# Performance work log

Measured on AMD Instinct MI355X. Metric: run time of the kernel, lower is better.

## Reference

```python
import jax, jax.numpy as jnp
import numpy as np

ALPHA = 0.2          # LeakyReLU negative slope
NEG_FILL = -9e15     # mask value used by the original module


def setup_inputs() -> dict:
    key = jax.random.key(0)
    k1, k2, k3, k4 = jax.random.split(key, 4)
    N, D, H, F = 4096, 512, 8, 64  # nhid*nheads == embedding_dim
    h = jax.random.normal(k1, (N, D), dtype=jnp.float32)
    adj = jax.random.randint(k2, (N, N), 0, 2, dtype=jnp.int32)
    # per-head linear projection weights (no bias) and attention vectors
    W = jax.random.normal(k3, (H, D, F), dtype=jnp.float32) * (1.0 / np.sqrt(D))
    a = jax.random.normal(k4, (H, 2 * F), dtype=jnp.float32) * 0.1
    return {"h": h, "adj": adj, "W": W, "a": a}


def reference(h, adj, W, a):
    H, D, F = W.shape
    N = h.shape[0]
    # per-head projection: [H, N, F]
    hp = jnp.einsum('nd,hdf->hnf', h, W)
    # score(i,j) = leakyrelu(a[:F].h_i + a[F:].h_j)  (decomposed broadcast-add,
    # same math as the original N*N concat construction)
    a_src, a_dst = a[:, :F], a[:, F:]
    f_src = jnp.einsum('hnf,hf->hn', hp, a_src)  # [H, N]
    f_dst = jnp.einsum('hnf,hf->hn', hp, a_dst)  # [H, N]
    e = jax.nn.leaky_relu(f_src[:, :, None] + f_dst[:, None, :], ALPHA)  # [H,N,N]
    e = jnp.where(adj[None] > 0, e, NEG_FILL)
    att = jax.nn.softmax(e, axis=-1)  # softmax over neighbors j (dim=1 in torch)
    out = jnp.einsum('hij,hjf->hif', att, hp)  # [H, N, F]
    # concat heads -> [N, H*F], then ELU
    out = jnp.transpose(out, (1, 0, 2)).reshape(N, H * F)
    return jax.nn.elu(out)
```

## Files before the change

### kernel.cpp

```cpp
#include <hip/hip_runtime.h>

#define NN 4096
#define DD 512
#define HH 8
#define FF 64
#define LRELU_ALPHA 0.2f
#define SP 72

typedef __attribute__((ext_vector_type(8))) short bf16x8;
typedef __attribute__((ext_vector_type(4))) float f32x4;

__device__ __forceinline__ float f4c(const float4& v, int k) {
    return k == 0 ? v.x : (k == 1 ? v.y : (k == 2 ? v.z : v.w));
}
__device__ __forceinline__ void f4s(float4& v, int k, float x) {
    if (k == 0) v.x = x; else if (k == 1) v.y = x; else if (k == 2) v.z = x; else v.w = x;
}
__device__ __forceinline__ unsigned short f2bf(float x) {
    unsigned u = __float_as_uint(x);
    return (unsigned short)((u + 0x7fffu + ((u >> 16) & 1u)) >> 16);
}
__device__ __forceinline__ float bf2f(unsigned short h) {
    return __uint_as_float(((unsigned)h) << 16);
}
__device__ __forceinline__ unsigned fkey(float x) {
    unsigned u = __float_as_uint(x);
    return (u & 0x80000000u) ? ~u : (u | 0x80000000u);
}
__device__ __forceinline__ float funkey(unsigned k) {
    unsigned u = (k & 0x80000000u) ? (k ^ 0x80000000u) : ~k;
    return __uint_as_float(u);
}

__global__ __launch_bounds__(256) void k_prep(const int* __restrict__ adj,
                                              const float* __restrict__ W,
                                              unsigned* __restrict__ adjw,
                                              unsigned short* __restrict__ wt_hi,
                                              unsigned short* __restrict__ wt_lo,
                                              unsigned* __restrict__ mxkey,
                                              float* __restrict__ hpsum) {
    __shared__ float tile[64][65];
    int b = blockIdx.x, t = threadIdx.x;
    if (b < 4096) {
        int lane = t & 63;
        #pragma unroll
        for (int i = 0; i < 16; i++) {
            int tid = ((b * 16 + i) << 8) + t;
            unsigned long long mask = __ballot(adj[tid] > 0);
            if (lane == 0) {
                int base = tid >> 5;
                adjw[base] = (unsigned)mask;
                adjw[base + 1] = (unsigned)(mask >> 32);
            }
        }
    } else if (b < 4160) {
        int idx = b - 4096;
        int h = idx >> 3;
        int d0 = (idx & 7) * 64;
        #pragma unroll
        for (int kidx = 0; kidx < 4; kidx++) {
            int id = t + 256 * kidx;
            int dd = id >> 4, f4i = (id & 15) * 4;
            float4 v = *(const float4*)(W + ((size_t)(h * DD + d0 + dd)) * FF + f4i);
            tile[dd][f4i] = v.x; tile[dd][f4i + 1] = v.y;
            tile[dd][f4i + 2] = v.z; tile[dd][f4i + 3] = v.w;
        }
        __syncthreads();
        int f = t >> 2, c = (t & 3) * 16;
        union { unsigned short s[16]; uint4 v[2]; } hb, lb;
        #pragma unroll
        for (int q = 0; q < 16; q++) {
            float v = tile[c + q][f];
            unsigned short hi = f2bf(v);
            hb.s[q] = hi;
            lb.s[q] = f2bf(v - bf2f(hi));
        }
        uint4* dh = (uint4*)(wt_hi + ((size_t)h * FF + f) * DD + d0 + c);
        uint4* dl = (uint4*)(wt_lo + ((size_t)h * FF + f) * DD + d0 + c);
        dh[0] = hb.v[0]; dh[1] = hb.v[1];
        dl[0] = lb.v[0]; dl[1] = lb.v[1];
    } else {
        if (t < 16) mxkey[t] = 0u;
        hpsum[t] = 0.f;
        hpsum[t + 256] = 0.f;
    }
}

__global__ __launch_bounds__(256) void k_hp_mfma(const float* __restrict__ hmat,
                                                 const unsigned short* __restrict__ whi,
                                                 const unsigned short* __restrict__ wlo,
                                                 const float* __restrict__ a,
                                                 unsigned short* __restrict__ hpT_hi,
                                                 float* __restrict__ fs,
                                                 float* __restrict__ fd,
                                                 float* __restrict__ hpsum,
                                                 unsigned* __restrict__ mxkey) {
    __shared__ char smem[4 * 64 * SP * 2];
    unsigned short* ah = (unsigned short*)smem;
    unsigned short* al = ah + 64 * SP;
    unsigned short* bh = al + 64 * SP;
    unsigned short* bl = bh + 64 * SP;

    int t = threadIdx.x;
    int h = blockIdx.y;
    int n0 = blockIdx.x * 64;
    int lane = t & 63;
    int w = t >> 6;
    int R0 = (w >> 1) * 32, F0 = (w & 1) * 32;
    int am = lane & 15, aq = lane >> 4;
    int sr = t >> 2, sc = (t & 3) * 16;

    const float* gha = hmat + (size_t)(n0 + sr) * DD;
    const unsigned short* gbh = whi + ((size_t)h * FF + sr) * DD;
    const unsigned short* gbl = wlo + ((size_t)h * FF + sr) * DD;

    f32x4 acc[2][2] = {};
    for (int kk = 0; kk < DD; kk += 64) {
        {
            float4 p0 = *(const float4*)(gha + kk + sc);
            float4 p1 = *(const float4*)(gha + kk + sc + 4);
            float4 p2 = *(const float4*)(gha + kk + sc + 8);
            float4 p3 = *(const float4*)(gha + kk + sc + 12);
            union { unsigned short s[16]; uint4 v[2]; } hb, lb;
            #pragma unroll
            for (int q = 0; q < 16; q++) {
                float v = q < 4 ? f4c(p0, q) : q < 8 ? f4c(p1, q - 4)
                          : q < 12 ? f4c(p2, q - 8) : f4c(p3, q - 12);
                unsigned short hi = f2bf(v);
                hb.s[q] = hi;
                lb.s[q] = f2bf(v - bf2f(hi));
            }
            *(uint4*)(ah + sr * SP + sc) = hb.v[0]; *(uint4*)(ah + sr * SP + sc + 8) = hb.v[1];
            *(uint4*)(al + sr * SP + sc) = lb.v[0]; *(uint4*)(al + sr * SP + sc + 8) = lb.v[1];
        }
        {
            const uint4* s2 = (const uint4*)(gbh + kk + sc);
            const uint4* s3 = (const uint4*)(gbl + kk + sc);
            uint4 w0 = s2[0], w1 = s2[1], x0 = s3[0], x1 = s3[1];
            *(uint4*)(bh + sr * SP + sc) = w0; *(uint4*)(bh + sr * SP + sc + 8) = w1;
            *(uint4*)(bl + sr * SP + sc) = x0; *(uint4*)(bl + sr * SP + sc + 8) = x1;
        }
        __syncthreads();
        #pragma unroll
        for (int k2 = 0; k2 < 2; k2++) {
            int ko = k2 * 32 + aq * 8;
            bf16x8 a0h = *(const bf16x8*)(ah + (R0 + am) * SP + ko);
            bf16x8 a1h = *(const bf16x8*)(ah + (R0 + 16 + am) * SP + ko);
            bf16x8 a0l = *(const bf16x8*)(al + (R0 + am) * SP + ko);
            bf16x8 a1l = *(const bf16x8*)(al + (R0 + 16 + am) * SP + ko);
            bf16x8 b0h = *(const bf16x8*)(bh + (F0 + am) * SP + ko);
            bf16x8 b1h = *(const bf16x8*)(bh + (F0 + 16 + am) * SP + ko);
            bf16x8 b0l = *(const bf16x8*)(bl + (F0 + am) * SP + ko);
            bf16x8 b1l = *(const bf16x8*)(bl + (F0 + 16 + am) * SP + ko);
            acc[0][0] = __builtin_amdgcn_mfma_f32_16x16x32_bf16(a0h, b0h, acc[0][0], 0, 0, 0);
            acc[0][1] = __builtin_amdgcn_mfma_f32_16x16x32_bf16(a0h, b1h, acc[0][1], 0, 0, 0);
            acc[1][0] = __builtin_amdgcn_mfma_f32_16x16x32_bf16(a1h, b0h, acc[1][0], 0, 0, 0);
            acc[1][1] = __builtin_amdgcn_mfma_f32_16x16x32_bf16(a1h, b1h, acc[1][1], 0, 0, 0);
            acc[0][0] = __builtin_amdgcn_mfma_f32_16x16x32_bf16(a0h, b0l, acc[0][0], 0, 0, 0);
            acc[0][1] = __builtin_amdgcn_mfma_f32_16x16x32_bf16(a0h, b1l, acc[0][1], 0, 0, 0);
            acc[1][0] = __builtin_amdgcn_mfma_f32_16x16x32_bf16(a1h, b0l, acc[1][0], 0, 0, 0);
            acc[1][1] = __builtin_amdgcn_mfma_f32_16x16x32_bf16(a1h, b1l, acc[1][1], 0, 0, 0);
            acc[0][0] = __builtin_amdgcn_mfma_f32_16x16x32_bf16(a0l, b0h, acc[0][0], 0, 0, 0);
            acc[0][1] = __builtin_amdgcn_mfma_f32_16x16x32_bf16(a0l, b1h, acc[0][1], 0, 0, 0);
            acc[1][0] = __builtin_amdgcn_mfma_f32_16x16x32_bf16(a1l, b0h, acc[1][0], 0, 0, 0);
            acc[1][1] = __builtin_amdgcn_mfma_f32_16x16x32_bf16(a1l, b1h, acc[1][1], 0, 0, 0);
        }
        __syncthreads();
    }

    unsigned* tt = (unsigned*)smem;
    float* rs = (float*)(smem + 17408);
    float* rd = rs + 256;
    float* ash = rd + 256;
    if (t < 128) ash[t] = a[h * 2 * FF + t];
    int col = lane & 15, rbase = (lane >> 4) * 4;
    #pragma unroll
    for (int m16 = 0; m16 < 2; m16++) {
        #pragma unroll
        for (int n16 = 0; n16 < 2; n16++) {
            #pragma unroll
            for (int r = 0; r < 4; r++) {
                int nl = R0 + m16 * 16 + rbase + r;
                int f = F0 + n16 * 16 + col;
                float v = acc[m16][n16][r];
                unsigned short hi = f2bf(v);
                unsigned short lo = f2bf(v - bf2f(hi));
                tt[f * 68 + nl] = (unsigned)hi | ((unsigned)lo << 16);
            }
        }
    }
    __syncthreads();
    {
        int f = t >> 2, c = (t & 3) * 16;
        union { unsigned short s[16]; uint4 v[2]; } hb;
        float csum = 0.f;
        #pragma unroll
        for (int q = 0; q < 16; q++) {
            unsigned u = tt[f * 68 + c + q];
            hb.s[q] = (unsigned short)(u & 0xffffu);
            csum += bf2f((unsigned short)(u & 0xffffu)) + bf2f((unsigned short)(u >> 16));
        }
        uint4* dh = (uint4*)(hpT_hi + ((size_t)h * FF + f) * NN + n0 + c);
        dh[0] = hb.v[0]; dh[1] = hb.v[1];
        csum += __shfl_xor(csum, 1);
        csum += __shfl_xor(csum, 2);
        if ((t & 3) == 0) unsafeAtomicAdd(hpsum + h * FF + f, csum);
    }
    {
        int n = t & 63, g = t >> 6;
        float fsp = 0.f, fdp = 0.f;
        #pragma unroll
        for (int q = 0; q < 16; q++) {
            int f = g * 16 + q;
            unsigned u = tt[f * 68 + n];
            float v = bf2f((unsigned short)(u & 0xffffu)) + bf2f((unsigned short)(u >> 16));
            fsp += v * ash[f];
            fdp += v * ash[64 + f];
        }
        rs[g * 64 + n] = fsp;
        rd[g * 64 + n] = fdp;
    }
    __syncthreads();
    if (t < 64) {
        float fdv = rd[t] + rd[64 + t] + rd[128 + t] + rd[192 + t];
        fs[(size_t)h * NN + n0 + t] = rs[t] + rs[64 + t] + rs[128 + t] + rs[192 + t];
        fd[(size_t)h * NN + n0 + t] = fdv;
        unsigned key = fkey(fdv);
        #pragma unroll
        for (int off = 32; off; off >>= 1) key = max(key, (unsigned)__shfl_xor((int)key, off));
        if (t == 0) atomicMax(mxkey + h, key);
    }
}

__global__ __launch_bounds__(256) void k_attn(const float* __restrict__ fs,
                                              const float* __restrict__ fd,
                                              const unsigned* __restrict__ mxkey,
                                              const unsigned* __restrict__ adjw,
                                              const unsigned short* __restrict__ hpT_hi,
                                              const float* __restrict__ hpsum,
                                              float* __restrict__ outp) {
    __shared__ unsigned short pa[2][32 * SP];
    __shared__ unsigned short hbh[2][64 * SP];
    __shared__ float fss[32], ms[32];

    int t = threadIdx.x;
    int h = blockIdx.y;
    int i0 = blockIdx.x * 32;
    int lane = t & 63;
    int w = t >> 6;

    const float LOG2E = 1.44269504f;
    float mfd = funkey(mxkey[h]);
    if (t < 32) {
        float fsv = fs[(size_t)h * NN + i0 + t];
        fss[t] = fsv;
        float s = fsv + mfd;
        float m = fmaxf(s, LRELU_ALPHA * s);
        ms[t] = m * LOG2E;
    }
    __syncthreads();

    int wr = t >> 3;
    int wc = (t & 7) * 8;
    int sr = t >> 2, sc = (t & 3) * 16;
    int R0 = (w >> 1) * 16, F0 = (w & 1) * 32;
    int am = lane & 15, aq = lane >> 4;
    f32x4 acc[2] = {};
    f32x4 accl = {};
    bf16x8 bones;
    #pragma unroll
    for (int i = 0; i < 8; i++) bones[i] = (short)0x3f80;

    const unsigned short* gH = hpT_hi + (size_t)h * FF * NN;
    const float* fdh = fd + (size_t)h * NN;
    float fsr = fss[wr], mr = ms[wr];

    auto produce = [&](int j0, int buf) {
        {
            const uint4* sh = (const uint4*)(gH + (size_t)sr * NN + j0 + sc);
            uint4 v0 = sh[0], v1 = sh[1];
            *(uint4*)(&hbh[buf][sr * SP + sc]) = v0;
            *(uint4*)(&hbh[buf][sr * SP + sc + 8]) = v1;
        }
        {
            unsigned word = adjw[(size_t)(i0 + wr) * (NN / 32) + ((j0 + wc) >> 5)];
            unsigned bits = word >> (wc & 31);
            union { unsigned u[4]; uint4 v; } wb;
            #pragma unroll
            for (int q = 0; q < 2; q++) {
                float4 fdv = *(const float4*)(fdh + j0 + wc + q * 4);
                unsigned eu[4];
                #pragma unroll
                for (int b = 0; b < 4; b++) {
                    float s = fsr + f4c(fdv, b);
                    float l = fmaxf(s, LRELU_ALPHA * s);
                    float e = __builtin_amdgcn_exp2f(__builtin_fmaf(l, LOG2E, -mr));
                    e = ((bits >> (q * 4 + b)) & 1u) ? e : 0.f;
                    eu[b] = __float_as_uint(e);
                }
                wb.u[q * 2]     = __builtin_amdgcn_perm(eu[1], eu[0], 0x07060302);
                wb.u[q * 2 + 1] = __builtin_amdgcn_perm(eu[3], eu[2], 0x07060302);
            }
            *(uint4*)(&pa[buf][wr * SP + wc]) = wb.v;
        }
    };

    produce(0, 0);
    __syncthreads();
    for (int j0 = 0; j0 < NN; j0 += 64) {
        int cur = (j0 >> 6) & 1;
        if (j0 + 64 < NN) produce(j0 + 64, cur ^ 1);
        #pragma unroll
        for (int k2 = 0; k2 < 2; k2++) {
            int ko = k2 * 32 + aq * 8;
            bf16x8 a0 = *(const bf16x8*)(&pa[cur][(R0 + am) * SP + ko]);
            bf16x8 b0 = *(const bf16x8*)(&hbh[cur][(F0 + am) * SP + ko]);
            bf16x8 b1 = *(const bf16x8*)(&hbh[cur][(F0 + 16 + am) * SP + ko]);
            acc[0] = __builtin_amdgcn_mfma_f32_16x16x32_bf16(a0, b0, acc[0], 0, 0, 0);
            acc[1] = __builtin_amdgcn_mfma_f32_16x16x32_bf16(a0, b1, acc[1], 0, 0, 0);
            accl   = __builtin_amdgcn_mfma_f32_16x16x32_bf16(a0, bones, accl, 0, 0, 0);
        }
        __syncthreads();
    }

    const float invN = 1.0f / NN;
    int col = lane & 15, rbase = (lane >> 4) * 4;
    #pragma unroll
    for (int r = 0; r < 4; r++) {
        int row = i0 + R0 + rbase + r;
        float l = accl[r];
        float rl = 1.f / l;
        #pragma unroll
        for (int n16 = 0; n16 < 2; n16++) {
            int f = F0 + n16 * 16 + col;
            float v;
            if (l > 0.f) v = acc[n16][r] * rl;
            else         v = hpsum[h * FF + f] * invN;
            v = v > 0.f ? v : __expf(v) - 1.f;
            outp[(size_t)row * (HH * FF) + h * FF + f] = v;
        }
    }
}

extern "C" void kernel_launch(void* const* d_in, const int* in_sizes, int n_in,
                              void* d_out, int out_size, void* d_ws, size_t ws_size,
                              hipStream_t stream) {
    const float* hmat = (const float*)d_in[0];
    const int*   adj  = (const int*)d_in[1];
    const float* W    = (const float*)d_in[2];
    const float* a    = (const float*)d_in[3];
    float* out = (float*)d_out;

    char* ws = (char*)d_ws;
    unsigned short* hpT_hi = (unsigned short*)(ws);
    unsigned*       adjw   = (unsigned*)(ws + (4u << 20));
    unsigned short* wt_hi  = (unsigned short*)(ws + (6u << 20));
    unsigned short* wt_lo  = (unsigned short*)(ws + (6u << 20) + (512u << 10));
    float* fs    = (float*)(ws + (7u << 20));
    float* fd    = (float*)(ws + (7u << 20) + (128u << 10));
    unsigned* mxkey = (unsigned*)(ws + (7u << 20) + (256u << 10));
    float* hpsum = (float*)(mxkey + 16);

    k_prep   <<<dim3(4161),          256, 0, stream>>>(adj, W, adjw, wt_hi, wt_lo,
                                                       mxkey, hpsum);
    k_hp_mfma<<<dim3(64, 8),         256, 0, stream>>>(hmat, wt_hi, wt_lo, a,
                                                       hpT_hi, fs, fd, hpsum, mxkey);
    k_attn   <<<dim3(NN / 32, HH),   256, 0, stream>>>(fs, fd, mxkey, adjw,
                                                       hpT_hi, hpsum, out);
}
```

Baseline: 192.0 us.

## Build P fragments in registers with scalar wave-wide adjacency masks

The adjacency bitmask is repacked in the prep kernel into per-wave 64-bit lane masks matching the MFMA fragment layout. The attention kernel then computes the exp-weight fragment directly in registers, with the mask applied as an SGPR operand to v_cndmask. This removes the shared-memory P buffer. LOG2E is folded into fs/fd upstream, and the LeakyReLU/max subtraction is rewritten as precomputed per-row constants. Each block now covers 64 rows, with every wave computing all 64 features, and output is written as float4. The cost is a more complex mask transpose in prep and higher register pressure from holding 16 mask words per iteration.

Result: slower. 219.5 us (+14.3%).

```diff
diff --git a/kernel.cpp b/kernel.cpp
--- a/kernel.cpp
+++ b/kernel.cpp
@@ -34,27 +34,42 @@
 
 __global__ __launch_bounds__(256) void k_prep(const int* __restrict__ adj,
                                               const float* __restrict__ W,
-                                              unsigned* __restrict__ adjw,
+                                              unsigned long long* __restrict__ adjm,
                                               unsigned short* __restrict__ wt_hi,
                                               unsigned short* __restrict__ wt_lo,
                                               unsigned* __restrict__ mxkey,
                                               float* __restrict__ hpsum) {
-    __shared__ float tile[64][65];
+    __shared__ unsigned long long shbuf[2080];
     int b = blockIdx.x, t = threadIdx.x;
-    if (b < 4096) {
-        int lane = t & 63;
-        #pragma unroll
-        for (int i = 0; i < 16; i++) {
-            int tid = ((b * 16 + i) << 8) + t;
-            unsigned long long mask = __ballot(adj[tid] > 0);
-            if (lane == 0) {
-                int base = tid >> 5;
-                adjw[base] = (unsigned)mask;
-                adjw[base + 1] = (unsigned)(mask >> 32);
+    if (b < 1024) {
+        int g = b >> 2, cq = b & 3;
+        int r0 = g * 16;
+        int lane = t & 63, wv = t >> 6;
+        unsigned long long (*w64)[17] = (unsigned long long(*)[17])shbuf;
+        for (int r = 0; r < 16; r++) {
+            #pragma unroll
+            for (int q = 0; q < 4; q++) {
+                int col = cq * 1024 + q * 256 + t;
+                unsigned long long m = __ballot(adj[(size_t)(r0 + r) * NN + col] > 0);
+                if (lane == 0) w64[r][q * 4 + wv] = m;
             }
         }
-    } else if (b < 4160) {
-        int idx = b - 4096;
+        __syncthreads();
+        for (int tt = wv; tt < 16; tt += 4) {
+            unsigned long long wbits = w64[lane & 15][tt];
+            unsigned long long my = 0;
+            #pragma unroll
+            for (int k = 0; k < 16; k++) {
+                int shv = 32 * (k >> 3) + 8 * (lane >> 4) + (k & 7);
+                unsigned long long bal = __ballot((unsigned)((wbits >> shv) & 1ULL));
+                if (lane == k) my = bal;
+            }
+            if (lane < 16)
+                adjm[((size_t)g * 64 + cq * 16 + tt) * 16 + lane] = my;
+        }
+    } else if (b < 1088) {
+        float (*tile)[65] = (float(*)[65])shbuf;
+        int idx = b - 1024;
         int h = idx >> 3;
         int d0 = (idx & 7) * 64;
         #pragma unroll
@@ -222,8 +237,9 @@
     }
     __syncthreads();
     if (t < 64) {
-        float fdv = rd[t] + rd[64 + t] + rd[128 + t] + rd[192 + t];
-        fs[(size_t)h * NN + n0 + t] = rs[t] + rs[64 + t] + rs[128 + t] + rs[192 + t];
+        const float LOG2E = 1.44269504f;
+        float fdv = (rd[t] + rd[64 + t] + rd[128 + t] + rd[192 + t]) * LOG2E;
+        fs[(size_t)h * NN + n0 + t] = (rs[t] + rs[64 + t] + rs[128 + t] + rs[192 + t]) * LOG2E;
         fd[(size_t)h * NN + n0 + t] = fdv;
         unsigned key = fkey(fdv);
         #pragma unroll
@@ -235,110 +251,139 @@
 __global__ __launch_bounds__(256) void k_attn(const float* __restrict__ fs,
                                               const float* __restrict__ fd,
                                               const unsigned* __restrict__ mxkey,
-                                              const unsigned* __restrict__ adjw,
+                                              const unsigned long long* __restrict__ adjm,
                                               const unsigned short* __restrict__ hpT_hi,
                                               const float* __restrict__ hpsum,
                                               float* __restrict__ outp) {
-    __shared__ unsigned short pa[2][32 * SP];
     __shared__ unsigned short hbh[2][64 * SP];
-    __shared__ float fss[32], ms[32];
 
     int t = threadIdx.x;
     int h = blockIdx.y;
-    int i0 = blockIdx.x * 32;
+    int i0 = blockIdx.x * 64;
     int lane = t & 63;
     int w = t >> 6;
-
-    const float LOG2E = 1.44269504f;
-    float mfd = funkey(mxkey[h]);
-    if (t < 32) {
-        float fsv = fs[(size_t)h * NN + i0 + t];
-        fss[t] = fsv;
-        float s = fsv + mfd;
-        float m = fmaxf(s, LRELU_ALPHA * s);
-        ms[t] = m * LOG2E;
-    }
-    __syncthreads();
-
-    int wr = t >> 3;
-    int wc = (t & 7) * 8;
+    int am = lane & 15, aq = lane >> 4;
     int sr = t >> 2, sc = (t & 3) * 16;
-    int R0 = (w >> 1) * 16, F0 = (w & 1) * 32;
-    int am = lane & 15, aq = lane >> 4;
-    f32x4 acc[2] = {};
-    f32x4 accl = {};
-    bf16x8 bones;
-    #pragma unroll
-    for (int i = 0; i < 8; i++) bones[i] = (short)0x3f80;
-
+
+    float mfdL = funkey(mxkey[h]);
+    float fsv = fs[(size_t)h * NN + i0 + w * 16 + am];
+    float sL = fsv + mfdL;
+    float mrL = fmaxf(sL, LRELU_ALPHA * sL);
+    float Ai = fsv - mrL;
+    float Ci = -0.8f * mrL;
+
+    int wu = __builtin_amdgcn_readfirstlane(w);
+    const unsigned long long* mbase = adjm + ((size_t)(blockIdx.x * 4 + wu) * 64) * 16;
     const unsigned short* gH = hpT_hi + (size_t)h * FF * NN;
     const float* fdh = fd + (size_t)h * NN;
-    float fsr = fss[wr], mr = ms[wr];
-
-    auto produce = [&](int j0, int buf) {
-        {
-            const uint4* sh = (const uint4*)(gH + (size_t)sr * NN + j0 + sc);
-            uint4 v0 = sh[0], v1 = sh[1];
-            *(uint4*)(&hbh[buf][sr * SP + sc]) = v0;
-            *(uint4*)(&hbh[buf][sr * SP + sc + 8]) = v1;
-        }
-        {
-            unsigned word = adjw[(size_t)(i0 + wr) * (NN / 32) + ((j0 + wc) >> 5)];
-            unsigned bits = word >> (wc & 31);
-            union { unsigned u[4]; uint4 v; } wb;
+
+    f32x4 acc[4] = {};
+    f32x4 accl = {};
+    bf16x8 ones;
+    #pragma unroll
+    for (int i = 0; i < 8; i++) ones[i] = (short)0x3f80;
+
+    auto stage_load = [&](int j0, uint4& v0, uint4& v1) {
+        const uint4* s = (const uint4*)(gH + (size_t)sr * NN + j0 + sc);
+        v0 = s[0]; v1 = s[1];
+    };
+    auto stage_write = [&](int buf, uint4 v0, uint4 v1) {
+        *(uint4*)(&hbh[buf][sr * SP + sc]) = v0;
+        *(uint4*)(&hbh[buf][sr * SP + sc + 8]) = v1;
+    };
+    auto fd_load = [&](int j0, float4* p) {
+        p[0] = *(const float4*)(fdh + j0 + aq * 8);
+        p[1] = *(const float4*)(fdh + j0 + aq * 8 + 4);
+        p[2] = *(const float4*)(fdh + j0 + 32 + aq * 8);
+        p[3] = *(const float4*)(fdh + j0 + 32 + aq * 8 + 4);
+    };
+    auto mkfrag = [&](float4 p0, float4 p1, const unsigned long long* mk, int off) -> bf16x8 {
+        unsigned eu[8];
+        #pragma unroll
+        for (int q = 0; q < 2; q++) {
+            float4 pv = q ? p1 : p0;
             #pragma unroll
-            for (int q = 0; q < 2; q++) {
-                float4 fdv = *(const float4*)(fdh + j0 + wc + q * 4);
-                unsigned eu[4];
-                #pragma unroll
-                for (int b = 0; b < 4; b++) {
-                    float s = fsr + f4c(fdv, b);
-                    float l = fmaxf(s, LRELU_ALPHA * s);
-                    float e = __builtin_amdgcn_exp2f(__builtin_fmaf(l, LOG2E, -mr));
-                    e = ((bits >> (q * 4 + b)) & 1u) ? e : 0.f;
-                    eu[b] = __float_as_uint(e);
-                }
-                wb.u[q * 2]     = __builtin_amdgcn_perm(eu[1], eu[0], 0x07060302);
-                wb.u[q * 2 + 1] = __builtin_amdgcn_perm(eu[3], eu[2], 0x07060302);
+            for (int bq = 0; bq < 4; bq++) {
+                float tv = Ai + f4c(pv, bq);
+                float uv = __builtin_fmaf(LRELU_ALPHA, tv, Ci);
+                float ev = __builtin_amdgcn_exp2f(fmaxf(tv, uv));
+                unsigned r;
+                asm("v_cndmask_b32 %0, 0, %1, %2"
+                    : "=v"(r) : "v"(ev), "s"(mk[off + q * 4 + bq]));
+                eu[q * 4 + bq] = r;
             }
-            *(uint4*)(&pa[buf][wr * SP + wc]) = wb.v;
-        }
+        }
+        union { unsigned u[4]; bf16x8 v; } pk;
+        pk.u[0] = __builtin_amdgcn_perm(eu[1], eu[0], 0x07060302);
+        pk.u[1] = __builtin_amdgcn_perm(eu[3], eu[2], 0x07060302);
+        pk.u[2] = __builtin_amdgcn_perm(eu[5], eu[4], 0x07060302);
+        pk.u[3] = __builtin_amdgcn_perm(eu[7], eu[6], 0x07060302);
+        return pk.v;
     };
 
-    produce(0, 0);
-    __syncthreads();
+    bf16x8 Pc0, Pc1;
+    {
+        uint4 v0, v1; float4 pf[4];
+        stage_load(0, v0, v1);
+        fd_load(0, pf);
+        unsigned long long mk[16];
+        #pragma unroll
+        for (int k = 0; k < 16; k++) mk[k] = mbase[k];
+        Pc0 = mkfrag(pf[0], pf[1], mk, 0);
+        Pc1 = mkfrag(pf[2], pf[3], mk, 8);
+        stage_write(0, v0, v1);
+        __syncthreads();
+    }
+
     for (int j0 = 0; j0 < NN; j0 += 64) {
         int cur = (j0 >> 6) & 1;
-        if (j0 + 64 < NN) produce(j0 + 64, cur ^ 1);
+        int jn = (j0 + 64) & (NN - 1);
+        uint4 v0, v1; float4 pf[4];
+        stage_load(jn, v0, v1);
+        fd_load(jn, pf);
+        unsigned long long mk[16];
+        #pragma unroll
+        for (int k = 0; k < 16; k++) mk[k] = mbase[(size_t)(jn >> 6) * 16 + k];
+
         #pragma unroll
         for (int k2 = 0; k2 < 2; k2++) {
             int ko = k2 * 32 + aq * 8;
-            bf16x8 a0 = *(const bf16x8*)(&pa[cur][(R0 + am) * SP + ko]);
-            bf16x8 b0 = *(const bf16x8*)(&hbh[cur][(F0 + am) * SP + ko]);
-            bf16x8 b1 = *(const bf16x8*)(&hbh[cur][(F0 + 16 + am) * SP + ko]);
-            acc[0] = __builtin_amdgcn_mfma_f32_16x16x32_bf16(a0, b0, acc[0], 0, 0, 0);
-            acc[1] = __builtin_amdgcn_mfma_f32_16x16x32_bf16(a0, b1, acc[1], 0, 0, 0);
-            accl   = __builtin_amdgcn_mfma_f32_16x16x32_bf16(a0, bones, accl, 0, 0, 0);
-        }
+            bf16x8 x0 = *(const bf16x8*)(&hbh[cur][(am)      * SP + ko]);
+            bf16x8 x1 = *(const bf16x8*)(&hbh[cur][(am + 16) * SP + ko]);
+            bf16x8 x2 = *(const bf16x8*)(&hbh[cur][(am + 32) * SP + ko]);
+            bf16x8 x3 = *(const bf16x8*)(&hbh[cur][(am + 48) * SP + ko]);
+            bf16x8 P = k2 ? Pc1 : Pc0;
+            acc[0] = __builtin_amdgcn_mfma_f32_16x16x32_bf16(x0, P, acc[0], 0, 0, 0);
+            acc[1] = __builtin_amdgcn_mfma_f32_16x16x32_bf16(x1, P, acc[1], 0, 0, 0);
+            acc[2] = __builtin_amdgcn_mfma_f32_16x16x32_bf16(x2, P, acc[2], 0, 0, 0);
+            acc[3] = __builtin_amdgcn_mfma_f32_16x16x32_bf16(x3, P, acc[3], 0, 0, 0);
+            accl   = __builtin_amdgcn_mfma_f32_16x16x32_bf16(ones, P, accl, 0, 0, 0);
+        }
+
+        stage_write(cur ^ 1, v0, v1);
+        Pc0 = mkfrag(pf[0], pf[1], mk, 0);
+        Pc1 = mkfrag(pf[2], pf[3], mk, 8);
         __syncthreads();
     }
 
     const float invN = 1.0f / NN;
-    int col = lane & 15, rbase = (lane >> 4) * 4;
+    float li = accl[0];
+    float rl = 1.f / li;
+    int row = i0 + w * 16 + am;
+    float* orow = outp + (size_t)row * (HH * FF) + h * FF;
     #pragma unroll
-    for (int r = 0; r < 4; r++) {
-        int row = i0 + R0 + rbase + r;
-        float l = accl[r];
-        float rl = 1.f / l;
-        #pragma unroll
-        for (int n16 = 0; n16 < 2; n16++) {
-            int f = F0 + n16 * 16 + col;
+    for (int mf = 0; mf < 4; mf++) {
+        float4 ov;
+        #pragma unroll
+        for (int r = 0; r < 4; r++) {
+            int f = mf * 16 + aq * 4 + r;
             float v;
-            if (l > 0.f) v = acc[n16][r] * rl;
-            else         v = hpsum[h * FF + f] * invN;
+            if (li > 0.f) v = acc[mf][r] * rl;
+            else          v = hpsum[h * FF + f] * invN;
             v = v > 0.f ? v : __expf(v) - 1.f;
-            outp[(size_t)row * (HH * FF) + h * FF + f] = v;
-        }
+            f4s(ov, r, v);
+        }
+        *(float4*)(orow + mf * 16 + aq * 4) = ov;
     }
 }
 
@@ -353,7 +398,7 @@
 
     char* ws = (char*)d_ws;
     unsigned short* hpT_hi = (unsigned short*)(ws);
-    unsigned*       adjw   = (unsigned*)(ws + (4u << 20));
+    unsigned long long* adjm = (unsigned long long*)(ws + (4u << 20));
     unsigned short* wt_hi  = (unsigned short*)(ws + (6u << 20));
     unsigned short* wt_lo  = (unsigned short*)(ws + (6u << 20) + (512u << 10));
     float* fs    = (float*)(ws + (7u << 20));
@@ -361,10 +406,10 @@
     unsigned* mxkey = (unsigned*)(ws + (7u << 20) + (256u << 10));
     float* hpsum = (float*)(mxkey + 16);
 
-    k_prep   <<<dim3(4161),          256, 0, stream>>>(adj, W, adjw, wt_hi, wt_lo,
+    k_prep   <<<dim3(1089),          256, 0, stream>>>(adj, W, adjm, wt_hi, wt_lo,
                                                        mxkey, hpsum);
     k_hp_mfma<<<dim3(64, 8),         256, 0, stream>>>(hmat, wt_hi, wt_lo, a,
                                                        hpT_hi, fs, fd, hpsum, mxkey);
-    k_attn   <<<dim3(NN / 32, HH),   256, 0, stream>>>(fs, fd, mxkey, adjw,
+    k_attn   <<<dim3(NN / 64, HH),   256, 0, stream>>>(fs, fd, mxkey, adjm,
                                                        hpT_hi, hpsum, out);
 }
```
